# Performance work log

Measured on AMD Instinct MI355X. Metric: run time of the kernel, lower is better.

## Reference

```python
import jax, jax.numpy as jnp
import numpy as np

B, D = 16384, 2048          # batch, input_dim
N_TOP, N_CLASS = 8, 16      # top labels, bottom labels per top (uniform, contiguous ids)

def setup_inputs() -> dict:
    key = jax.random.key(0)
    k1, k2, k3, k4, k5 = jax.random.split(key, 5)
    INIT = 0.2  # matches init_weight uniform(-0.2, 0.2)
    return {
        "features": jax.random.normal(k1, (B, D), dtype=jnp.float32),
        "top_W": jax.random.uniform(k2, (N_TOP, D), minval=-INIT, maxval=INIT, dtype=jnp.float32),
        "top_b": jax.random.uniform(k3, (N_TOP,), minval=-INIT, maxval=INIT, dtype=jnp.float32),
        "bottom_W": jax.random.uniform(k4, (N_TOP, D, N_CLASS), minval=-INIT, maxval=INIT, dtype=jnp.float32),
        "bottom_b": jax.random.uniform(k5, (N_TOP, N_CLASS), minval=-INIT, maxval=INIT, dtype=jnp.float32),
    }

def reference(features, top_W, top_b, bottom_W, bottom_b):
    # dropout p=0.0 -> identity
    # top gate: linear + sigmoid, (b, n_top)
    top_scores = jax.nn.sigmoid(features @ top_W.T + top_b)
    # all per-top-label expert linears as one batched GEMM: (b, n_top, n_class)
    bottom_logits = jnp.einsum('bd,tdc->btc', features, bottom_W) + bottom_b
    bottom_scores = jax.nn.softmax(bottom_logits, axis=-1)
    # scatter-combine: bottom ids of top i are contiguous [i*N_CLASS, (i+1)*N_CLASS),
    # so the column scatter is a reshape. (b, n_bottom_labels)
    final_scores = (top_scores[:, :, None] * bottom_scores).reshape(features.shape[0], N_TOP * N_CLASS)
    return final_scores
```

## Files before the change

### kernel.cpp

```cpp
#include <hip/hip_runtime.h>


#define D_DIM 2048
#define NTILE 9
#define M_ROWS 64
#define STEP_HALFS 6144
#define NSTEPS 64

using f32x4 = float __attribute__((ext_vector_type(4)));
using half8 = _Float16 __attribute__((ext_vector_type(8)));
using fp16x2 = __fp16 __attribute__((ext_vector_type(2)));

__global__ void prep_weights(const float* __restrict__ topW,
                             const float* __restrict__ botW,
                             _Float16* __restrict__ S) {
    int idx = blockIdx.x * blockDim.x + threadIdx.x;
    if (idx >= NSTEPS * NTILE * 64) return;
    int lane = idx & 63;
    int tmp  = idx >> 6;
    int nt   = tmp % NTILE;
    int KS   = tmp / NTILE;
    int n     = nt * 16 + (lane & 15);
    int kbase = KS * 32 + (lane >> 4) * 8;

    _Float16 v[8];
    #pragma unroll
    for (int j = 0; j < 8; j++) {
        int k = kbase + j;
        float x = 0.0f;
        if (n < 8) {
            x = topW[n * D_DIM + k];
        } else if (n < 136) {
            int t = (n - 8) >> 4, c = (n - 8) & 15;
            x = botW[(t * D_DIM + k) * 16 + c];
        }
        v[j] = (_Float16)x;
    }
    *(half8*)(S + (size_t)KS * STEP_HALFS + (size_t)(nt * 64 + lane) * 8) = *(half8*)v;
}

static __device__ __forceinline__ half8 pack_af(f32x4 a, f32x4 b) {
    fp16x2 p0 = __builtin_amdgcn_cvt_pkrtz(a[0], a[1]);
    fp16x2 p1 = __builtin_amdgcn_cvt_pkrtz(a[2], a[3]);
    fp16x2 p2 = __builtin_amdgcn_cvt_pkrtz(b[0], b[1]);
    fp16x2 p3 = __builtin_amdgcn_cvt_pkrtz(b[2], b[3]);
    half8 r;
    r[0] = (_Float16)p0[0]; r[1] = (_Float16)p0[1];
    r[2] = (_Float16)p1[0]; r[3] = (_Float16)p1[1];
    r[4] = (_Float16)p2[0]; r[5] = (_Float16)p2[1];
    r[6] = (_Float16)p3[0]; r[7] = (_Float16)p3[1];
    return r;
}

#define GL4(dst, voff, sbase, IMM)                                         \
    asm volatile("global_load_dwordx4 %0, %1, %2 offset:%3"                \
                 : "=v"(dst) : "v"(voff), "s"(sbase), "i"(IMM))

#define VWAIT(N) do {                                                      \
        asm volatile("s_waitcnt vmcnt(%0)" :: "i"(N) : "memory");          \
        __builtin_amdgcn_sched_barrier(0);                                 \
    } while (0)

#define SB() __builtin_amdgcn_sched_barrier(0)
#define BAR() do { __builtin_amdgcn_s_barrier();                           \
                   __builtin_amdgcn_sched_barrier(0); } while (0)

typedef __attribute__((address_space(1))) const void gv_t;
typedef __attribute__((address_space(3))) void lv_t;

__global__ __launch_bounds__(256, 2) void hc_fused(
        const float* __restrict__ feat, const _Float16* __restrict__ Bsw,
        const float* __restrict__ top_b, const float* __restrict__ bot_b,
        float* __restrict__ out) {
    __shared__ _Float16 bufB[3][STEP_HALFS];
    __shared__ float red[4][16][148];

    const int tid  = threadIdx.x;
    const int lane = tid & 63, wave = tid >> 6;
    const int quad = lane >> 4, low = lane & 15;
    const int rowg0 = blockIdx.x * M_ROWS + wave * 16;

    const unsigned long long sA = (unsigned long long)feat;
    const unsigned aBase = (unsigned)(((unsigned)(rowg0 + low) * D_DIM + quad * 8) * 4);

    f32x4 acc[NTILE];
    #pragma unroll
    for (int i = 0; i < NTILE; i++) acc[i] = (f32x4)0.0f;

    f32x4 aX0, aX1, aY0, aY1;

#define STAGE(GSRC, SLOT) do {                                             \
        const _Float16* g_ = (GSRC) + (size_t)tid * 8;                     \
        _Pragma("unroll")                                                  \
        for (int r_ = 0; r_ < 3; r_++) {                                   \
            __builtin_amdgcn_global_load_lds(                              \
                (gv_t*)(g_ + r_ * 2048),                                   \
                (lv_t*)&bufB[SLOT][(unsigned)(r_ * 256 + wave * 64) * 8],  \
                16, 0, 0);                                                 \
        }                                                                  \
    } while (0)

#define COMPUTE(SLOT, AL0, AL1) do {                                       \
        const _Float16* Lp_ = &bufB[SLOT][(unsigned)lane * 8];             \
        half8 f0_ = *(const half8*)(Lp_);                                  \
        half8 f1_ = *(const half8*)(Lp_ +  512);                           \
        half8 f2_ = *(const half8*)(Lp_ + 1024);                           \
        half8 f3_ = *(const half8*)(Lp_ + 1536);                           \
        half8 f4_ = *(const half8*)(Lp_ + 2048);                           \
        half8 f5_ = *(const half8*)(Lp_ + 2560);                           \
        half8 f6_ = *(const half8*)(Lp_ + 3072);                           \
        half8 f7_ = *(const half8*)(Lp_ + 3584);                           \
        half8 f8_ = *(const half8*)(Lp_ + 4096);                           \
        const half8 af_ = pack_af(AL0, AL1);                               \
        acc[0] = __builtin_amdgcn_mfma_f32_16x16x32_f16(af_, f0_, acc[0], 0, 0, 0); \
        acc[1] = __builtin_amdgcn_mfma_f32_16x16x32_f16(af_, f1_, acc[1], 0, 0, 0); \
        acc[2] = __builtin_amdgcn_mfma_f32_16x16x32_f16(af_, f2_, acc[2], 0, 0, 0); \
        acc[3] = __builtin_amdgcn_mfma_f32_16x16x32_f16(af_, f3_, acc[3], 0, 0, 0); \
        acc[4] = __builtin_amdgcn_mfma_f32_16x16x32_f16(af_, f4_, acc[4], 0, 0, 0); \
        acc[5] = __builtin_amdgcn_mfma_f32_16x16x32_f16(af_, f5_, acc[5], 0, 0, 0); \
        acc[6] = __builtin_amdgcn_mfma_f32_16x16x32_f16(af_, f6_, acc[6], 0, 0, 0); \
        acc[7] = __builtin_amdgcn_mfma_f32_16x16x32_f16(af_, f7_, acc[7], 0, 0, 0); \
        acc[8] = __builtin_amdgcn_mfma_f32_16x16x32_f16(af_, f8_, acc[8], 0, 0, 0); \
    } while (0)

    STAGE(Bsw, 0); SB();
    GL4(aX0, aBase, sA, 0);   GL4(aX1, aBase, sA, 16);  SB();
    STAGE(Bsw + STEP_HALFS, 1); SB();
    GL4(aY0, aBase, sA, 128); GL4(aY1, aBase, sA, 144); SB();

    unsigned aoffX = aBase + 256;
    unsigned aoffY = aBase + 384;
    const _Float16* gS = Bsw + (size_t)2 * STEP_HALFS;
    int se = 0, so = 1;

    for (int i = 0; i < 31; ++i) {
        VWAIT(5); BAR();
        COMPUTE(se, aX0, aX1);
        SB();
        int we = se - 1; if (we < 0) we += 3;
        STAGE(gS, we); gS += STEP_HALFS; SB();
        GL4(aX0, aoffX, sA, 0); GL4(aX1, aoffX, sA, 16); aoffX += 256; SB();
        se = we;
        VWAIT(5); BAR();
        COMPUTE(so, aY0, aY1);
        SB();
        int wo = so - 1; if (wo < 0) wo += 3;
        STAGE(gS, wo); gS += STEP_HALFS; SB();
        GL4(aY0, aoffY, sA, 0); GL4(aY1, aoffY, sA, 16); aoffY += 256; SB();
        so = wo;
    }
    VWAIT(5); BAR(); COMPUTE(se, aX0, aX1);
    VWAIT(0); BAR(); COMPUTE(so, aY0, aY1);

#undef STAGE
#undef COMPUTE

    #pragma unroll
    for (int nt = 0; nt < NTILE; nt++) {
        #pragma unroll
        for (int r = 0; r < 4; r++) {
            red[wave][quad * 4 + r][nt * 16 + low] = acc[nt][r];
        }
    }
    __syncthreads();

    {
        const int row = lane & 15;
        const int q2  = lane >> 4;
        #pragma unroll
        for (int tt = 0; tt < 2; tt++) {
            const int t = q2 * 2 + tt;
            float zt = red[wave][row][t] + top_b[t];
            const float sig = 1.0f / (1.0f + __expf(-zt));

            float z[16];
            float zmax = -1e30f;
            #pragma unroll
            for (int c = 0; c < 16; c++) {
                float v = red[wave][row][8 + t * 16 + c] + bot_b[t * 16 + c];
                z[c] = v;
                zmax = fmaxf(zmax, v);
            }
            float s = 0.0f;
            #pragma unroll
            for (int c = 0; c < 16; c++) { z[c] = __expf(z[c] - zmax); s += z[c]; }
            const float scale = sig / s;

            float* o = out + (size_t)(rowg0 + row) * 128 + t * 16;
            #pragma unroll
            for (int c = 0; c < 16; c += 4) {
                f32x4 v = { z[c] * scale, z[c+1] * scale, z[c+2] * scale, z[c+3] * scale };
                *(f32x4*)(o + c) = v;
            }
        }
    }
}

extern "C" void kernel_launch(void* const* d_in, const int* in_sizes, int n_in,
                              void* d_out, int out_size, void* d_ws, size_t ws_size,
                              hipStream_t stream) {
    const float* feat  = (const float*)d_in[0];
    const float* topW  = (const float*)d_in[1];
    const float* topB  = (const float*)d_in[2];
    const float* botW  = (const float*)d_in[3];
    const float* botB  = (const float*)d_in[4];
    float* out = (float*)d_out;
    _Float16* Bsw = (_Float16*)d_ws;

    prep_weights<<<(NSTEPS * NTILE * 64 + 255) / 256, 256, 0, stream>>>(topW, botW, Bsw);
    hc_fused<<<16384 / M_ROWS, 256, 0, stream>>>(feat, Bsw, topB, botB, out);
}
```

Baseline: 223.1 us.

## Split K across wave pairs with 512-thread blocks and three-deep A prefetch

Doubles the block to 8 waves, and each pair of waves splits the 2048-wide reduction into two halves. Each step now stages both halves' weight tiles into LDS, and the two partial accumulators are summed in the shared-memory epilogue. The main loop is fully unrolled with three rotating A-register sets so features are prefetched three steps ahead instead of two. The intent is more memory-level parallelism per CU and half as many barrier-separated steps per block. The cost is one block per CU with larger LDS use, and extra reduction work in the epilogue.

After: 215.7 us. 3.3% less time.

```diff
diff --git a/kernel.cpp b/kernel.cpp
--- a/kernel.cpp
+++ b/kernel.cpp
@@ -4,8 +4,9 @@
 #define D_DIM 2048
 #define NTILE 9
 #define M_ROWS 64
-#define STEP_HALFS 6144
-#define NSTEPS 64
+#define NSTEPS 32
+#define STEP_BYTES 18432
+#define SLOT_HALFS 9216
 
 using f32x4 = float __attribute__((ext_vector_type(4)));
 using half8 = _Float16 __attribute__((ext_vector_type(8)));
@@ -15,13 +16,15 @@
                              const float* __restrict__ botW,
                              _Float16* __restrict__ S) {
     int idx = blockIdx.x * blockDim.x + threadIdx.x;
-    if (idx >= NSTEPS * NTILE * 64) return;
+    if (idx >= NSTEPS * 2 * NTILE * 64) return;
     int lane = idx & 63;
     int tmp  = idx >> 6;
     int nt   = tmp % NTILE;
-    int KS   = tmp / NTILE;
+    int skg  = tmp / NTILE;
+    int kg   = skg & 1;
+    int s    = skg >> 1;
     int n     = nt * 16 + (lane & 15);
-    int kbase = KS * 32 + (lane >> 4) * 8;
+    int kbase = kg * 1024 + s * 32 + (lane >> 4) * 8;
 
     _Float16 v[8];
     #pragma unroll
@@ -36,7 +39,8 @@
         }
         v[j] = (_Float16)x;
     }
-    *(half8*)(S + (size_t)KS * STEP_HALFS + (size_t)(nt * 64 + lane) * 8) = *(half8*)v;
+    *(half8*)(S + (size_t)s * SLOT_HALFS + (size_t)kg * 4608
+                + (size_t)(nt * 64 + lane) * 8) = *(half8*)v;
 }
 
 static __device__ __forceinline__ half8 pack_af(f32x4 a, f32x4 b) {
@@ -68,40 +72,51 @@
 typedef __attribute__((address_space(1))) const void gv_t;
 typedef __attribute__((address_space(3))) void lv_t;
 
-__global__ __launch_bounds__(256, 2) void hc_fused(
+__global__ __launch_bounds__(512, 1) void hc_fused(
         const float* __restrict__ feat, const _Float16* __restrict__ Bsw,
         const float* __restrict__ top_b, const float* __restrict__ bot_b,
         float* __restrict__ out) {
-    __shared__ _Float16 bufB[3][STEP_HALFS];
-    __shared__ float red[4][16][148];
+    __shared__ _Float16 bufB[3][SLOT_HALFS];
+    __shared__ float red[8][16][148];
 
     const int tid  = threadIdx.x;
     const int lane = tid & 63, wave = tid >> 6;
     const int quad = lane >> 4, low = lane & 15;
-    const int rowg0 = blockIdx.x * M_ROWS + wave * 16;
+    const int mrow = wave >> 1, kg = wave & 1;
+    const int rowg0 = blockIdx.x * M_ROWS + mrow * 16;
 
     const unsigned long long sA = (unsigned long long)feat;
-    const unsigned aBase = (unsigned)(((unsigned)(rowg0 + low) * D_DIM + quad * 8) * 4);
+    const unsigned vA = (unsigned)(((unsigned)(rowg0 + low) * D_DIM
+                                    + kg * 1024 + quad * 8) * 4);
+
+    const char* gB = (const char*)Bsw;
+    const char* lB = (const char*)&bufB[0][0];
 
     f32x4 acc[NTILE];
     #pragma unroll
     for (int i = 0; i < NTILE; i++) acc[i] = (f32x4)0.0f;
 
-    f32x4 aX0, aX1, aY0, aY1;
-
-#define STAGE(GSRC, SLOT) do {                                             \
-        const _Float16* g_ = (GSRC) + (size_t)tid * 8;                     \
-        _Pragma("unroll")                                                  \
-        for (int r_ = 0; r_ < 3; r_++) {                                   \
-            __builtin_amdgcn_global_load_lds(                              \
-                (gv_t*)(g_ + r_ * 2048),                                   \
-                (lv_t*)&bufB[SLOT][(unsigned)(r_ * 256 + wave * 64) * 8],  \
-                16, 0, 0);                                                 \
+    f32x4 aX0, aX1, aY0, aY1, aZ0, aZ1;
+
+#define STAGE(SLOT, KS) do {                                               \
+        const char* g0_ = gB + (KS) * STEP_BYTES + wave * 2304             \
+                             + (unsigned)lane * 16;                        \
+        const char* l0_ = lB + (SLOT) * STEP_BYTES + wave * 2304;          \
+        __builtin_amdgcn_global_load_lds((gv_t*)(g0_),                     \
+                                         (lv_t*)(l0_), 16, 0, 0);          \
+        __builtin_amdgcn_global_load_lds((gv_t*)(g0_ + 1024),              \
+                                         (lv_t*)(l0_ + 1024), 16, 0, 0);   \
+        if (low16_) {                                                      \
+            __builtin_amdgcn_global_load_lds((gv_t*)(g0_ + 2048),          \
+                                             (lv_t*)(l0_ + 2048), 16, 0, 0);\
         }                                                                  \
     } while (0)
-
-#define COMPUTE(SLOT, AL0, AL1) do {                                       \
-        const _Float16* Lp_ = &bufB[SLOT][(unsigned)lane * 8];             \
+    const bool low16_ = (lane < 16);
+
+    const _Float16* Lb = (const _Float16*)lB + kg * 4608 + lane * 8;
+
+#define COMPUTE(KS, A0r, A1r) do {                                         \
+        const _Float16* Lp_ = Lb + ((KS) % 3) * SLOT_HALFS;                \
         half8 f0_ = *(const half8*)(Lp_);                                  \
         half8 f1_ = *(const half8*)(Lp_ +  512);                           \
         half8 f2_ = *(const half8*)(Lp_ + 1024);                           \
@@ -111,7 +126,7 @@
         half8 f6_ = *(const half8*)(Lp_ + 3072);                           \
         half8 f7_ = *(const half8*)(Lp_ + 3584);                           \
         half8 f8_ = *(const half8*)(Lp_ + 4096);                           \
-        const half8 af_ = pack_af(AL0, AL1);                               \
+        const half8 af_ = pack_af(A0r, A1r);                               \
         acc[0] = __builtin_amdgcn_mfma_f32_16x16x32_f16(af_, f0_, acc[0], 0, 0, 0); \
         acc[1] = __builtin_amdgcn_mfma_f32_16x16x32_f16(af_, f1_, acc[1], 0, 0, 0); \
         acc[2] = __builtin_amdgcn_mfma_f32_16x16x32_f16(af_, f2_, acc[2], 0, 0, 0); \
@@ -123,37 +138,38 @@
         acc[8] = __builtin_amdgcn_mfma_f32_16x16x32_f16(af_, f8_, acc[8], 0, 0, 0); \
     } while (0)
 
-    STAGE(Bsw, 0); SB();
-    GL4(aX0, aBase, sA, 0);   GL4(aX1, aBase, sA, 16);  SB();
-    STAGE(Bsw + STEP_HALFS, 1); SB();
-    GL4(aY0, aBase, sA, 128); GL4(aY1, aBase, sA, 144); SB();
-
-    unsigned aoffX = aBase + 256;
-    unsigned aoffY = aBase + 384;
-    const _Float16* gS = Bsw + (size_t)2 * STEP_HALFS;
-    int se = 0, so = 1;
-
-    for (int i = 0; i < 31; ++i) {
-        VWAIT(5); BAR();
-        COMPUTE(se, aX0, aX1);
-        SB();
-        int we = se - 1; if (we < 0) we += 3;
-        STAGE(gS, we); gS += STEP_HALFS; SB();
-        GL4(aX0, aoffX, sA, 0); GL4(aX1, aoffX, sA, 16); aoffX += 256; SB();
-        se = we;
-        VWAIT(5); BAR();
-        COMPUTE(so, aY0, aY1);
-        SB();
-        int wo = so - 1; if (wo < 0) wo += 3;
-        STAGE(gS, wo); gS += STEP_HALFS; SB();
-        GL4(aY0, aoffY, sA, 0); GL4(aY1, aoffY, sA, 16); aoffY += 256; SB();
-        so = wo;
-    }
-    VWAIT(5); BAR(); COMPUTE(se, aX0, aX1);
-    VWAIT(0); BAR(); COMPUTE(so, aY0, aY1);
-
+#define STEP(KS, W, A0r, A1r) do {                                         \
+        VWAIT(W); BAR();                                                   \
+        COMPUTE(KS, A0r, A1r); SB();                                       \
+        if ((KS) + 2 < NSTEPS) { STAGE(((KS) + 2) % 3, (KS) + 2); } SB();  \
+        if ((KS) + 3 < NSTEPS) {                                           \
+            GL4(A0r, vA, sA, ((KS) + 3) * 128);                            \
+            GL4(A1r, vA, sA, ((KS) + 3) * 128 + 16);                       \
+        } SB();                                                            \
+    } while (0)
+
+    STAGE(0, 0); SB();
+    GL4(aX0, vA, sA,   0); GL4(aX1, vA, sA,  16); SB();
+    GL4(aY0, vA, sA, 128); GL4(aY1, vA, sA, 144); SB();
+    STAGE(1, 1); SB();
+    GL4(aZ0, vA, sA, 256); GL4(aZ1, vA, sA, 272); SB();
+
+    STEP( 0, 7, aX0, aX1);  STEP( 1, 7, aY0, aY1);  STEP( 2, 7, aZ0, aZ1);
+    STEP( 3, 7, aX0, aX1);  STEP( 4, 7, aY0, aY1);  STEP( 5, 7, aZ0, aZ1);
+    STEP( 6, 7, aX0, aX1);  STEP( 7, 7, aY0, aY1);  STEP( 8, 7, aZ0, aZ1);
+    STEP( 9, 7, aX0, aX1);  STEP(10, 7, aY0, aY1);  STEP(11, 7, aZ0, aZ1);
+    STEP(12, 7, aX0, aX1);  STEP(13, 7, aY0, aY1);  STEP(14, 7, aZ0, aZ1);
+    STEP(15, 7, aX0, aX1);  STEP(16, 7, aY0, aY1);  STEP(17, 7, aZ0, aZ1);
+    STEP(18, 7, aX0, aX1);  STEP(19, 7, aY0, aY1);  STEP(20, 7, aZ0, aZ1);
+    STEP(21, 7, aX0, aX1);  STEP(22, 7, aY0, aY1);  STEP(23, 7, aZ0, aZ1);
+    STEP(24, 7, aX0, aX1);  STEP(25, 7, aY0, aY1);  STEP(26, 7, aZ0, aZ1);
+    STEP(27, 7, aX0, aX1);  STEP(28, 7, aY0, aY1);  STEP(29, 7, aZ0, aZ1);
+    STEP(30, 5, aX0, aX1);
+    STEP(31, 0, aY0, aY1);
+
+#undef STEP
+#undef COMPUTE
 #undef STAGE
-#undef COMPUTE
 
     #pragma unroll
     for (int nt = 0; nt < NTILE; nt++) {
@@ -165,33 +181,34 @@
     __syncthreads();
 
     {
-        const int row = lane & 15;
-        const int q2  = lane >> 4;
-        #pragma unroll
-        for (int tt = 0; tt < 2; tt++) {
-            const int t = q2 * 2 + tt;
-            float zt = red[wave][row][t] + top_b[t];
-            const float sig = 1.0f / (1.0f + __expf(-zt));
-
-            float z[16];
-            float zmax = -1e30f;
-            #pragma unroll
-            for (int c = 0; c < 16; c++) {
-                float v = red[wave][row][8 + t * 16 + c] + bot_b[t * 16 + c];
-                z[c] = v;
-                zmax = fmaxf(zmax, v);
-            }
-            float s = 0.0f;
-            #pragma unroll
-            for (int c = 0; c < 16; c++) { z[c] = __expf(z[c] - zmax); s += z[c]; }
-            const float scale = sig / s;
-
-            float* o = out + (size_t)(rowg0 + row) * 128 + t * 16;
-            #pragma unroll
-            for (int c = 0; c < 16; c += 4) {
-                f32x4 v = { z[c] * scale, z[c+1] * scale, z[c+2] * scale, z[c+3] * scale };
-                *(f32x4*)(o + c) = v;
-            }
+        const int row = tid >> 3;
+        const int top = tid & 7;
+        const int mg  = row >> 4;
+        const int r16 = row & 15;
+
+        float zt = red[mg * 2][r16][top] + red[mg * 2 + 1][r16][top] + top_b[top];
+        const float sig = 1.0f / (1.0f + __expf(-zt));
+
+        float z[16];
+        float zmax = -1e30f;
+        #pragma unroll
+        for (int c = 0; c < 16; c++) {
+            float v = red[mg * 2][r16][8 + top * 16 + c]
+                    + red[mg * 2 + 1][r16][8 + top * 16 + c]
+                    + bot_b[top * 16 + c];
+            z[c] = v;
+            zmax = fmaxf(zmax, v);
+        }
+        float s = 0.0f;
+        #pragma unroll
+        for (int c = 0; c < 16; c++) { z[c] = __expf(z[c] - zmax); s += z[c]; }
+        const float scale = sig / s;
+
+        float* o = out + (size_t)(blockIdx.x * M_ROWS + row) * 128 + top * 16;
+        #pragma unroll
+        for (int c = 0; c < 16; c += 4) {
+            f32x4 v = { z[c] * scale, z[c+1] * scale, z[c+2] * scale, z[c+3] * scale };
+            *(f32x4*)(o + c) = v;
         }
     }
 }
@@ -207,6 +224,6 @@
     float* out = (float*)d_out;
     _Float16* Bsw = (_Float16*)d_ws;
 
-    prep_weights<<<(NSTEPS * NTILE * 64 + 255) / 256, 256, 0, stream>>>(topW, botW, Bsw);
-    hc_fused<<<16384 / M_ROWS, 256, 0, stream>>>(feat, Bsw, topB, botB, out);
-}
+    prep_weights<<<(NSTEPS * 2 * NTILE * 64 + 255) / 256, 256, 0, stream>>>(topW, botW, Bsw);
+    hc_fused<<<16384 / M_ROWS, 512, 0, stream>>>(feat, Bsw, topB, botB, out);
+}
```
